# Kernel tuning notes

Hardware: AMD Instinct MI355X
Metric: run time of the kernel (lower is better)

## Reference

```python
import jax, jax.numpy as jnp
import numpy as np

S, B, I, H = 2048, 128, 128, 128


def setup_inputs() -> dict:
    key = jax.random.key(0)
    k1, k2, k3, k4, k5 = jax.random.split(key, 5)
    x = jax.random.normal(k1, (S, B, I), dtype=jnp.float32)
    V = jax.random.normal(k2, (4 * H, I), dtype=jnp.float32) * 0.05
    W = jax.random.normal(k3, (4 * H, H), dtype=jnp.float32) * 0.05
    b = jax.random.normal(k4, (4 * H,), dtype=jnp.float32) * 0.05
    b2 = jax.random.normal(k5, (4 * H,), dtype=jnp.float32) * 0.05
    return {"x": x, "V": V, "W": W, "b": b, "b2": b2}


def reference(x, V, W, b, b2):
    seq_len, batch, _ = x.shape
    hid = W.shape[1]
    # Precompute input contribution for all timesteps (same math, batched matmul)
    xg = jnp.einsum('sbi,gi->sbg', x, V) + b + b2  # (S, B, 4H)

    def step(carry, xg_t):
        h, c = carry
        gates = xg_t + h @ W.T  # (B, 4H)
        i, f, g, o = jnp.split(gates, 4, axis=1)
        i = jax.nn.sigmoid(i)
        f = jax.nn.sigmoid(f)
        g = jnp.tanh(g)
        o = jax.nn.sigmoid(o)
        c = f * c + i * g
        h = o * jnp.tanh(c)
        return (h, c), h

    h0 = jnp.zeros((batch, hid), dtype=x.dtype)
    c0 = jnp.zeros((batch, hid), dtype=x.dtype)
    (h_T, c_T), hs = jax.lax.scan(step, (h0, c0), xg)  # hs: (S, B, H)
    # Original torch.cat of h_t.unsqueeze(1) along dim 0 -> (S*B, 1, H)
    h_seq = hs.reshape(seq_len * batch, 1, hid)
    return h_seq, h_T[:, None, :], c_T[:, None, :]
```

## Files before the change

kernel.cpp:

```cpp
#include <hip/hip_runtime.h>
#include <hip/hip_bf16.h>
#include <hip/hip_fp16.h>


#define S_LEN 2048
#define BATCH 128
#define HID   128
#define G4    512

typedef _Float16 h2_t __attribute__((ext_vector_type(2)));
typedef _Float16 h8_t __attribute__((ext_vector_type(8)));
typedef float    f4_t __attribute__((ext_vector_type(4)));

__global__ __launch_bounds__(256, 2)
void xg_gemm(const float* __restrict__ x, const float* __restrict__ V,
             const float* __restrict__ b, const float* __restrict__ b2,
             __half* __restrict__ xg)
{
    __shared__ h8_t As[128 * 16];
    __shared__ h8_t Bs[128 * 16];

    const int t  = threadIdx.x;
    const int m0 = blockIdx.y * 128;
    const int n0 = blockIdx.x * 128;

#pragma unroll
    for (int r = 0; r < 8; ++r) {
        int id  = t + 256 * r;
        int row = id >> 4;
        int j   = id & 15;
        const float4* gx = (const float4*)(x + (long)(m0 + row) * 128 + j * 8);
        float4 a0 = gx[0], a1 = gx[1];
        h8_t ha = { (_Float16)a0.x, (_Float16)a0.y, (_Float16)a0.z, (_Float16)a0.w,
                    (_Float16)a1.x, (_Float16)a1.y, (_Float16)a1.z, (_Float16)a1.w };
        As[row * 16 + (j ^ (row & 15))] = ha;
        const float4* gv = (const float4*)(V + (long)(n0 + row) * 128 + j * 8);
        float4 b0 = gv[0], b1 = gv[1];
        h8_t hb = { (_Float16)b0.x, (_Float16)b0.y, (_Float16)b0.z, (_Float16)b0.w,
                    (_Float16)b1.x, (_Float16)b1.y, (_Float16)b1.z, (_Float16)b1.w };
        Bs[row * 16 + (j ^ (row & 15))] = hb;
    }
    __syncthreads();

    const int w    = t >> 6;
    const int lane = t & 63;
    const int m    = lane & 15;
    const int quad = lane >> 4;

    f4_t acc[2][8];
#pragma unroll
    for (int i = 0; i < 2; ++i)
#pragma unroll
        for (int j = 0; j < 8; ++j) acc[i][j] = (f4_t)0.f;

#pragma unroll
    for (int ks = 0; ks < 4; ++ks) {
        int ch = ks * 4 + quad;
        h8_t a0 = As[(w * 32      + m) * 16 + (ch ^ m)];
        h8_t a1 = As[(w * 32 + 16 + m) * 16 + (ch ^ m)];
#pragma unroll
        for (int nt = 0; nt < 8; ++nt) {
            h8_t bf = Bs[(nt * 16 + m) * 16 + (ch ^ m)];
            acc[0][nt] = __builtin_amdgcn_mfma_f32_16x16x32_f16(a0, bf, acc[0][nt], 0, 0, 0);
            acc[1][nt] = __builtin_amdgcn_mfma_f32_16x16x32_f16(a1, bf, acc[1][nt], 0, 0, 0);
        }
    }

#pragma unroll
    for (int nt = 0; nt < 8; ++nt) {
        int col = n0 + nt * 16 + m;
        float bias = b[col] + b2[col];
#pragma unroll
        for (int mi = 0; mi < 2; ++mi) {
#pragma unroll
            for (int rg = 0; rg < 4; ++rg) {
                long mrow = (long)(m0 + w * 32 + mi * 16 + quad * 4 + rg);
                xg[mrow * G4 + col] = __float2half(acc[mi][nt][rg] + bias);
            }
        }
    }
}

__device__ __forceinline__ float fsig(float x) {
    return __builtin_amdgcn_rcpf(1.f + __expf(-x));
}
__device__ __forceinline__ float ftanh(float x) {
    return 1.f - 2.f * __builtin_amdgcn_rcpf(1.f + __expf(2.f * x));
}
__device__ __forceinline__ void bar() {
    asm volatile("s_waitcnt lgkmcnt(0)" ::: "memory");
    __builtin_amdgcn_s_barrier();
    asm volatile("" ::: "memory");
}

#if __has_builtin(__builtin_amdgcn_fdot2)
#define FDOT2(a, b, c) __builtin_amdgcn_fdot2((a), (b), (c), false)
#else
__device__ __forceinline__ float FDOT2(h2_t a, h2_t b, float c) {
    return c + (float)a[0] * (float)b[0] + (float)a[1] * (float)b[1];
}
#endif

template <int CTRL>
__device__ __forceinline__ float dpp_mov_f(float x) {
#if __has_builtin(__builtin_amdgcn_mov_dpp)
    int xi = __builtin_bit_cast(int, x);
    int yi = __builtin_amdgcn_mov_dpp(xi, CTRL, 0xf, 0xf, true);
    return __builtin_bit_cast(float, yi);
#else
    return x;
#endif
}
#define QP_XOR1  0xB1
#define QP_XOR2  0x4E
#define QP_BC0   0x00
#define QP_BC1   0x55
#define QP_BC2   0xAA
#define QP_BC3   0xFF

__global__ __launch_bounds__(512, 2)
void lstm_scan(const __half* __restrict__ xg, const float* __restrict__ W,
               float* __restrict__ out)
{
    const int bidx = blockIdx.x;
    const int t    = threadIdx.x;
    const int hid  = t >> 2;
    const int kq   = t & 3;

    __shared__ __align__(16) __half h_buf[2][HID];

    h2_t wr[4][16];
#pragma unroll
    for (int r = 0; r < 4; ++r) {
        const float4* Wp = (const float4*)(W + (long)(hid + 128 * r) * 128 + kq * 32);
#pragma unroll
        for (int q = 0; q < 8; ++q) {
            float4 v = Wp[q];
            wr[r][2 * q]     = h2_t{ (_Float16)v.x, (_Float16)v.y };
            wr[r][2 * q + 1] = h2_t{ (_Float16)v.z, (_Float16)v.w };
        }
    }

    if (t < HID) h_buf[0][t] = __float2half(0.f);
    __syncthreads();

    const __half* xgp = xg + (long)bidx * G4 + hid + kq * 128;
    const long step_stride = (long)BATCH * G4;

    float p0 = __half2float(xgp[0]);
    float p1 = __half2float(xgp[step_stride]);

    float c = 0.f, hlast = 0.f;
    const float ascale = (kq == 2) ? 2.f : 1.f;
    float* out_h = out + (long)bidx * HID;
    const long SBH = (long)S_LEN * BATCH * HID;

    for (int s = 0; s < S_LEN; ++s) {
        long soff = (long)((s + 2 < S_LEN) ? s + 2 : S_LEN - 1) * step_stride;
        float nx = __half2float(xgp[soff]);
        float xv = p0;

        const float4* hp = (const float4*)(&h_buf[s & 1][0]);
        float acc0 = 0.f, acc1 = 0.f, acc2 = 0.f, acc3 = 0.f;
#pragma unroll
        for (int q = 0; q < 4; ++q) {
            union { float4 f; h2_t h[4]; } u;
            u.f = hp[kq * 4 + q];
#pragma unroll
            for (int j = 0; j < 4; ++j) {
                h2_t hh = u.h[j];
                int cidx = q * 4 + j;
                acc0 = FDOT2(wr[0][cidx], hh, acc0);
                acc1 = FDOT2(wr[1][cidx], hh, acc1);
                acc2 = FDOT2(wr[2][cidx], hh, acc2);
                acc3 = FDOT2(wr[3][cidx], hh, acc3);
            }
        }
        acc0 += dpp_mov_f<QP_XOR1>(acc0);  acc0 += dpp_mov_f<QP_XOR2>(acc0);
        acc1 += dpp_mov_f<QP_XOR1>(acc1);  acc1 += dpp_mov_f<QP_XOR2>(acc1);
        acc2 += dpp_mov_f<QP_XOR1>(acc2);  acc2 += dpp_mov_f<QP_XOR2>(acc2);
        acc3 += dpp_mov_f<QP_XOR1>(acc3);  acc3 += dpp_mov_f<QP_XOR2>(acc3);

        float mydot = acc0;
        mydot = (kq == 1) ? acc1 : mydot;
        mydot = (kq == 2) ? acc2 : mydot;
        mydot = (kq == 3) ? acc3 : mydot;
        float pre = mydot + xv;
        float act = ascale * fsig(ascale * pre) - (ascale - 1.f);

        float gi = dpp_mov_f<QP_BC0>(act);
        float gf = dpp_mov_f<QP_BC1>(act);
        float gg = dpp_mov_f<QP_BC2>(act);
        float go = dpp_mov_f<QP_BC3>(act);

        c = gf * c + gi * gg;
        float h = go * ftanh(c);
        hlast = h;

        if (kq == 0) {
            h_buf[(s + 1) & 1][hid] = __float2half(h);
            out_h[(long)s * (BATCH * HID) + hid] = h;
        }
        bar();

        p0 = p1; p1 = nx;
    }

    if (kq == 0) {
        out[SBH + (long)bidx * HID + hid]                     = hlast;
        out[SBH + (long)BATCH * HID + (long)bidx * HID + hid] = c;
    }
}

extern "C" void kernel_launch(void* const* d_in, const int* in_sizes, int n_in,
                              void* d_out, int out_size, void* d_ws, size_t ws_size,
                              hipStream_t stream) {
    const float* x  = (const float*)d_in[0];
    const float* V  = (const float*)d_in[1];
    const float* W  = (const float*)d_in[2];
    const float* b  = (const float*)d_in[3];
    const float* b2 = (const float*)d_in[4];
    float* out = (float*)d_out;
    __half* xg = (__half*)d_ws;

    dim3 g1(G4 / 128, (S_LEN * BATCH) / 128);
    xg_gemm<<<g1, dim3(256), 0, stream>>>(x, V, b, b2, xg);
    lstm_scan<<<dim3(BATCH), dim3(512), 0, stream>>>(xg, W, out);
}
```

Before: 1.429 ms.

## Compute recurrent h@W^T per step with MFMA instead of fdot2 and DPP reductions

The per-timestep recurrent matvec moves from per-thread fdot2 accumulation plus quad DPP reductions and broadcasts to 16x16x32 f16 MFMA ops. Each wave holds a 16-row slice of all four gate blocks in registers as MFMA A operands, and the h vector is fed as the B operand, so every output column is the same vector. Each lane then computes all four gate activations for one hidden unit itself, which removes the cross-lane shuffles. The cost is that 15 of the 16 MFMA output columns are redundant, and the MFMA issue-to-result latency now sits on the serial per-step critical path.

After: 1.449 ms. Within noise of the previous version (+1.4%).

```diff
diff --git a/kernel.cpp b/kernel.cpp
--- a/kernel.cpp
+++ b/kernel.cpp
@@ -93,120 +93,101 @@
     asm volatile("" ::: "memory");
 }
 
-#if __has_builtin(__builtin_amdgcn_fdot2)
-#define FDOT2(a, b, c) __builtin_amdgcn_fdot2((a), (b), (c), false)
-#else
-__device__ __forceinline__ float FDOT2(h2_t a, h2_t b, float c) {
-    return c + (float)a[0] * (float)b[0] + (float)a[1] * (float)b[1];
-}
-#endif
-
-template <int CTRL>
-__device__ __forceinline__ float dpp_mov_f(float x) {
-#if __has_builtin(__builtin_amdgcn_mov_dpp)
-    int xi = __builtin_bit_cast(int, x);
-    int yi = __builtin_amdgcn_mov_dpp(xi, CTRL, 0xf, 0xf, true);
-    return __builtin_bit_cast(float, yi);
-#else
-    return x;
-#endif
-}
-#define QP_XOR1  0xB1
-#define QP_XOR2  0x4E
-#define QP_BC0   0x00
-#define QP_BC1   0x55
-#define QP_BC2   0xAA
-#define QP_BC3   0xFF
-
 __global__ __launch_bounds__(512, 2)
 void lstm_scan(const __half* __restrict__ xg, const float* __restrict__ W,
                float* __restrict__ out)
 {
     const int bidx = blockIdx.x;
     const int t    = threadIdx.x;
-    const int hid  = t >> 2;
-    const int kq   = t & 3;
+    const int w    = t >> 6;
+    const int lane = t & 63;
+    const int col  = lane & 15;
+    const int quad = lane >> 4;
+    const int rg   = col & 3;
+    const int hid  = 16 * w + quad * 4 + rg;
 
     __shared__ __align__(16) __half h_buf[2][HID];
 
-    h2_t wr[4][16];
-#pragma unroll
-    for (int r = 0; r < 4; ++r) {
-        const float4* Wp = (const float4*)(W + (long)(hid + 128 * r) * 128 + kq * 32);
-#pragma unroll
-        for (int q = 0; q < 8; ++q) {
-            float4 v = Wp[q];
-            wr[r][2 * q]     = h2_t{ (_Float16)v.x, (_Float16)v.y };
-            wr[r][2 * q + 1] = h2_t{ (_Float16)v.z, (_Float16)v.w };
+    h8_t a[4][4];
+#pragma unroll
+    for (int g = 0; g < 4; ++g) {
+        const float* Wr = W + (long)(g * 128 + 16 * w + col) * 128 + quad * 8;
+#pragma unroll
+        for (int kc = 0; kc < 4; ++kc) {
+            const float4* wp = (const float4*)(Wr + kc * 32);
+            float4 v0 = wp[0], v1 = wp[1];
+            a[g][kc] = h8_t{ (_Float16)v0.x, (_Float16)v0.y, (_Float16)v0.z, (_Float16)v0.w,
+                             (_Float16)v1.x, (_Float16)v1.y, (_Float16)v1.z, (_Float16)v1.w };
         }
     }
 
     if (t < HID) h_buf[0][t] = __float2half(0.f);
     __syncthreads();
 
-    const __half* xgp = xg + (long)bidx * G4 + hid + kq * 128;
+    const __half* xp = xg + (long)bidx * G4 + hid;
     const long step_stride = (long)BATCH * G4;
 
-    float p0 = __half2float(xgp[0]);
-    float p1 = __half2float(xgp[step_stride]);
+    __half p0[4], p1[4];
+#pragma unroll
+    for (int g = 0; g < 4; ++g) {
+        p0[g] = xp[g * 128];
+        p1[g] = xp[step_stride + g * 128];
+    }
 
     float c = 0.f, hlast = 0.f;
-    const float ascale = (kq == 2) ? 2.f : 1.f;
     float* out_h = out + (long)bidx * HID;
     const long SBH = (long)S_LEN * BATCH * HID;
 
+    const bool sel1 = (col & 1) != 0;
+    const bool sel2 = (col & 2) != 0;
+
     for (int s = 0; s < S_LEN; ++s) {
         long soff = (long)((s + 2 < S_LEN) ? s + 2 : S_LEN - 1) * step_stride;
-        float nx = __half2float(xgp[soff]);
-        float xv = p0;
-
-        const float4* hp = (const float4*)(&h_buf[s & 1][0]);
-        float acc0 = 0.f, acc1 = 0.f, acc2 = 0.f, acc3 = 0.f;
-#pragma unroll
-        for (int q = 0; q < 4; ++q) {
-            union { float4 f; h2_t h[4]; } u;
-            u.f = hp[kq * 4 + q];
-#pragma unroll
-            for (int j = 0; j < 4; ++j) {
-                h2_t hh = u.h[j];
-                int cidx = q * 4 + j;
-                acc0 = FDOT2(wr[0][cidx], hh, acc0);
-                acc1 = FDOT2(wr[1][cidx], hh, acc1);
-                acc2 = FDOT2(wr[2][cidx], hh, acc2);
-                acc3 = FDOT2(wr[3][cidx], hh, acc3);
-            }
-        }
-        acc0 += dpp_mov_f<QP_XOR1>(acc0);  acc0 += dpp_mov_f<QP_XOR2>(acc0);
-        acc1 += dpp_mov_f<QP_XOR1>(acc1);  acc1 += dpp_mov_f<QP_XOR2>(acc1);
-        acc2 += dpp_mov_f<QP_XOR1>(acc2);  acc2 += dpp_mov_f<QP_XOR2>(acc2);
-        acc3 += dpp_mov_f<QP_XOR1>(acc3);  acc3 += dpp_mov_f<QP_XOR2>(acc3);
-
-        float mydot = acc0;
-        mydot = (kq == 1) ? acc1 : mydot;
-        mydot = (kq == 2) ? acc2 : mydot;
-        mydot = (kq == 3) ? acc3 : mydot;
-        float pre = mydot + xv;
-        float act = ascale * fsig(ascale * pre) - (ascale - 1.f);
-
-        float gi = dpp_mov_f<QP_BC0>(act);
-        float gf = dpp_mov_f<QP_BC1>(act);
-        float gg = dpp_mov_f<QP_BC2>(act);
-        float go = dpp_mov_f<QP_BC3>(act);
-
-        c = gf * c + gi * gg;
-        float h = go * ftanh(c);
-        hlast = h;
-
-        if (kq == 0) {
-            h_buf[(s + 1) & 1][hid] = __float2half(h);
-            out_h[(long)s * (BATCH * HID) + hid] = h;
+        __half nx[4];
+#pragma unroll
+        for (int g = 0; g < 4; ++g) nx[g] = xp[soff + g * 128];
+
+        const h8_t* hb = (const h8_t*)(&h_buf[s & 1][0]);
+
+        f4_t acc0 = (f4_t)0.f, acc1 = (f4_t)0.f, acc2 = (f4_t)0.f, acc3 = (f4_t)0.f;
+#pragma unroll
+        for (int kc = 0; kc < 4; ++kc) {
+            h8_t bf = hb[kc * 4 + quad];
+            acc0 = __builtin_amdgcn_mfma_f32_16x16x32_f16(a[0][kc], bf, acc0, 0, 0, 0);
+            acc1 = __builtin_amdgcn_mfma_f32_16x16x32_f16(a[1][kc], bf, acc1, 0, 0, 0);
+            acc2 = __builtin_amdgcn_mfma_f32_16x16x32_f16(a[2][kc], bf, acc2, 0, 0, 0);
+            acc3 = __builtin_amdgcn_mfma_f32_16x16x32_f16(a[3][kc], bf, acc3, 0, 0, 0);
+        }
+
+        float v01, v23;
+        v01 = sel1 ? acc0[1] : acc0[0];  v23 = sel1 ? acc0[3] : acc0[2];
+        float pi = (sel2 ? v23 : v01) + __half2float(p0[0]);
+        v01 = sel1 ? acc1[1] : acc1[0];  v23 = sel1 ? acc1[3] : acc1[2];
+        float pf = (sel2 ? v23 : v01) + __half2float(p0[1]);
+        v01 = sel1 ? acc2[1] : acc2[0];  v23 = sel1 ? acc2[3] : acc2[2];
+        float pg = (sel2 ? v23 : v01) + __half2float(p0[2]);
+        v01 = sel1 ? acc3[1] : acc3[0];  v23 = sel1 ? acc3[3] : acc3[2];
+        float po = (sel2 ? v23 : v01) + __half2float(p0[3]);
+
+        float ia = fsig(pi);
+        float fa = fsig(pf);
+        float ga = ftanh(pg);
+        float oa = fsig(po);
+        c = fa * c + ia * ga;
+        float hv = oa * ftanh(c);
+        hlast = hv;
+
+        if (col < 4) {
+            h_buf[(s + 1) & 1][hid] = __float2half(hv);
+            out_h[(long)s * (BATCH * HID) + hid] = hv;
         }
         bar();
 
-        p0 = p1; p1 = nx;
-    }
-
-    if (kq == 0) {
+#pragma unroll
+        for (int g = 0; g < 4; ++g) { p0[g] = p1[g]; p1[g] = nx[g]; }
+    }
+
+    if (col < 4) {
         out[SBH + (long)bidx * HID + hid]                     = hlast;
         out[SBH + (long)BATCH * HID + (long)bidx * HID + hid] = c;
     }
```
